# Optimization experiments

Hardware: AMD Instinct MI355X
Metric: run time of the kernel (lower is better)

Reference implementation:

```python
import jax, jax.numpy as jnp
import numpy as np

# Config matching init_kwargs: input_shape=(C,T,H,W)=(512,32,14,14), window_size=9, n_heads=8
B, C, T, H, W = 2, 512, 32, 14, 14
N, K = 8, 9
CI = C // N              # per-head inter channels (64)
P = (K - 1) // 2         # symmetric temporal zero-pad so S == T


def setup_inputs() -> dict:
    key = jax.random.key(0)
    ks = jax.random.split(key, 7)
    s = 0.02
    return {
        "x":  jax.random.normal(ks[0], (B, C, T, H, W), jnp.float32),
        # per-head 1x1x1 conv (Linear3d) weights/biases, stacked over heads
        "Wq": jax.random.normal(ks[1], (N, CI, C), jnp.float32) * s,
        "bq": jax.random.normal(ks[2], (N, CI), jnp.float32) * s,
        "Wk": jax.random.normal(ks[3], (N, CI, C), jnp.float32) * s,
        "bk": jax.random.normal(ks[4], (N, CI), jnp.float32) * s,
        "Wv": jax.random.normal(ks[5], (N, CI, C), jnp.float32) * s,
        "bv": jax.random.normal(ks[6], (N, CI), jnp.float32) * s,
    }


def reference(x, Wq, bq, Wk, bk, Wv, bv):
    # x: (B, C, T, H, W). Dropout (p=0.25) is inference-mode identity.
    Bx, Cx, Tx, Hx, Wd = x.shape
    HW = Hx * Wd
    xf = x.reshape(Bx, Cx, Tx, HW)

    # Queries: every original frame is the center of its own window -> project x directly.
    q = jnp.einsum('bctp,nic->bnitp', xf, Wq) + bq[None, :, :, None, None]  # (B,N,ci,T,HW)

    # Keys/values on temporally zero-padded input (Pad3d gives S == T windows).
    xp = jnp.pad(xf, ((0, 0), (0, 0), (P, P), (0, 0)))  # (B,C,T+K-1,HW)
    k = jnp.einsum('bctp,nic->bnitp', xp, Wk) + bk[None, :, :, None, None]
    v = jnp.einsum('bctp,nic->bnitp', xp, Wv) + bv[None, :, :, None, None]

    # Sliding windows over padded time: window s covers padded frames s..s+K-1
    win = jnp.arange(Tx)[:, None] + jnp.arange(K)[None, :]  # (T,K)
    kw = k[:, :, :, win]  # (B,N,ci,T,K,HW)
    vw = v[:, :, :, win].reshape(Bx, N, CI, Tx, K * HW)

    # alpha[b,n,t,p,m] = sum_i q[b,n,i,t,p] * k_win[b,n,i,t,m]; softmax over keys m
    alpha = jnp.einsum('bnitp,bnitkm->bntpkm', q, kw).reshape(Bx, N, Tx, HW, K * HW)
    alpha = jax.nn.softmax(alpha, axis=-1)

    # y = alpha @ value -> (B,N,ci,T,HW); head concat is channel-major reshape
    y = jnp.einsum('bntpm,bnitm->bnitp', alpha, vw)
    z = y.reshape(Bx, Cx, Tx, Hx, Wd) + x  # residual
    return z
```

## Files before the change

kernel.cpp:

```cpp
#include <hip/hip_runtime.h>
#include <hip/hip_bf16.h>
#include <stdint.h>
#include <cstddef>

#define BB  2
#define CC  512
#define TT  32
#define HWP 196
#define NH  8
#define KWIN 9
#define CID 64
#define PPAD 4
#define TP  40
#define MTOT 12544
#define NTOT 1536
#define VSLOT 224
#define LOG2E 1.44269504f

typedef unsigned short u16;
typedef unsigned int   u32;
typedef __attribute__((ext_vector_type(8))) short short8;
typedef __attribute__((ext_vector_type(4))) float floatx4;

__device__ __forceinline__ u16 f2bf(float f) {
    u32 u = __float_as_uint(f);
    u32 r = (u + 0x7fffu + ((u >> 16) & 1u)) >> 16;
    return (u16)r;
}
__device__ __forceinline__ u32 pack2bf(float a, float b) {
    return (u32)f2bf(a) | ((u32)f2bf(b) << 16);
}
__device__ __forceinline__ u32 packtrunc(float a, float b) {
    return __builtin_amdgcn_perm(__float_as_uint(b), __float_as_uint(a), 0x07060302u);
}
__device__ __forceinline__ float fexp2(float x) {
    return __builtin_amdgcn_exp2f(x);
}
__device__ __forceinline__ void gload16(const u16* g, u16* l) {
    __builtin_amdgcn_global_load_lds(
        (const __attribute__((address_space(1))) u32*)g,
        (__attribute__((address_space(3))) u32*)l, 16, 0, 0);
}

__global__ __launch_bounds__(256) void prep_transpose(
    const float* __restrict__ x, u16* __restrict__ xt,
    const float* __restrict__ Wq, const float* __restrict__ Wk,
    const float* __restrict__ Wv, u16* __restrict__ Wbf,
    const float* __restrict__ bk, const float* __restrict__ bv,
    u16* __restrict__ Kout, u16* __restrict__ Vtp)
{
    __shared__ float T[64 * 197];
    int bxg = blockIdx.x;
    int tid = threadIdx.x;

    if (bxg < BB * TT * 8) {
        int bx = bxg;
        int ct = bx & 7; bx >>= 3;
        int t = bx & 31;
        int b = bx >> 5;
        const float* src = x + ((size_t)(b * CC + ct * 64) * TT + t) * HWP;
        for (int i = tid; i < 64 * 49; i += 256) {
            int c = i / 49;
            int p4 = i - c * 49;
            float4 v = *(const float4*)(src + (size_t)c * (TT * HWP) + p4 * 4);
            float* Tp = &T[c * 197 + p4 * 4];
            Tp[0] = v.x; Tp[1] = v.y; Tp[2] = v.z; Tp[3] = v.w;
        }
        __syncthreads();
        u16* dst = xt + (size_t)((b * TT + t) * HWP) * CC + ct * 64;
        for (int i = tid; i < HWP * 8; i += 256) {
            int p = i >> 3;
            int c0 = (i & 7) * 8;
            u32 w[4];
            #pragma unroll
            for (int k = 0; k < 4; k++)
                w[k] = pack2bf(T[(c0 + 2 * k) * 197 + p],
                               T[(c0 + 2 * k + 1) * 197 + p]);
            *(uint4*)(dst + (size_t)p * CC + c0) = *(uint4*)w;
        }
        return;
    }

    int id = (bxg - BB * TT * 8) * 256 + tid;
    const int wtot = NTOT * CC / 2;
    const int kper = 2 * NH * 8 * HWP * 32;
    const int vper = 2 * NH * 8 * 64 * (VSLOT/2);
    if (id < wtot) {
        int c2 = id & 255;
        int oc = id >> 8;
        int kind = oc >> 9;
        int idx = oc & 511;
        const float* src = (kind == 0 ? Wq : (kind == 1 ? Wk : Wv)) + (size_t)idx * CC + c2 * 2;
        ((u32*)Wbf)[id] = pack2bf(src[0], src[1]);
    } else if (id < wtot + kper) {
        int i = id - wtot;
        int ci2 = i & 31; i >>= 5;
        int p = i % HWP;  i /= HWP;
        int fr = i & 7;   i >>= 3;
        int head = i & 7;
        int b = i >> 3;
        int tp = fr < 4 ? fr : fr + 32;
        const float* bias = bk + head * CID + ci2 * 2;
        size_t addr = (((size_t)(b * NH + head) * TP + tp) * HWP + p) * 32 + ci2;
        ((u32*)Kout)[addr] = pack2bf(bias[0], bias[1]);
    } else if (id < wtot + kper + vper) {
        int i = id - wtot - kper;
        int s2 = i % (VSLOT/2); i /= (VSLOT/2);
        int ci = i & 63; i >>= 6;
        int fr = i & 7;  i >>= 3;
        int head = i & 7;
        int b = i >> 3;
        int tp = fr < 4 ? fr : fr + 32;
        float bias = bv[head * CID + ci];
        size_t addr = (((size_t)(b * NH + head) * TP + tp) * 64 + ci) * (VSLOT/2) + s2;
        ((u32*)Vtp)[addr] = pack2bf(bias, bias);
    }
}

__global__ __launch_bounds__(512) void proj_gemm2(
    const u16* __restrict__ xt, const u16* __restrict__ Wbf,
    const float* __restrict__ bq, const float* __restrict__ bk,
    const float* __restrict__ bv,
    u16* __restrict__ Qout, u16* __restrict__ Kout, u16* __restrict__ Vplain)
{
    __shared__ u16 sA[128 * 64];
    __shared__ u16 sB[256 * 64];

    int bx = blockIdx.x;
    int nb = bx % 6;
    int mt = bx / 6;
    int tid = threadIdx.x;
    int wave = tid >> 6, lane = tid & 63, quad = lane >> 4, l15 = lane & 15;
    int wm = wave >> 2, wn = wave & 3;
    int mbase = mt * 128 + wm * 64;
    int nbase = nb * 256 + wn * 64;

    int lr = lane >> 3;
    int sw = ((lane & 7) * 8) ^ (lr << 3);

    floatx4 acc[4][4];
    #pragma unroll
    for (int ms = 0; ms < 4; ms++)
        #pragma unroll
        for (int ns = 0; ns < 4; ns++)
            acc[ms][ns] = (floatx4){0.f, 0.f, 0.f, 0.f};

    const u16* abase = xt + (size_t)(mt * 128) * CC;
    const u16* bbase = Wbf + (size_t)(nb * 256) * CC;

    for (int kc = 0; kc < 8; kc++) {
        __syncthreads();
        #pragma unroll
        for (int i = 0; i < 2; i++) {
            int rbase = wave * 16 + i * 8;
            gload16(abase + (size_t)(rbase + lr) * CC + kc * 64 + sw,
                    &sA[rbase * 64]);
        }
        #pragma unroll
        for (int i = 0; i < 4; i++) {
            int rbase = wave * 32 + i * 8;
            gload16(bbase + (size_t)(rbase + lr) * CC + kc * 64 + sw,
                    &sB[rbase * 64]);
        }
        __syncthreads();

        #pragma unroll
        for (int kk = 0; kk < 2; kk++) {
            int swr = (kk * 32 + quad * 8) ^ ((l15 & 7) << 3);
            short8 af[4], bf[4];
            #pragma unroll
            for (int ms = 0; ms < 4; ms++)
                af[ms] = *(const short8*)&sA[(wm * 64 + ms * 16 + l15) * 64 + swr];
            #pragma unroll
            for (int ns = 0; ns < 4; ns++)
                bf[ns] = *(const short8*)&sB[(wn * 64 + ns * 16 + l15) * 64 + swr];
            #pragma unroll
            for (int ms = 0; ms < 4; ms++)
                #pragma unroll
                for (int ns = 0; ns < 4; ns++)
                    acc[ms][ns] = __builtin_amdgcn_mfma_f32_16x16x32_bf16(
                        af[ms], bf[ns], acc[ms][ns], 0, 0, 0);
        }
    }

    float biasv[4];
    #pragma unroll
    for (int ns = 0; ns < 4; ns++) {
        int n = nbase + ns * 16 + l15;
        int kind = n >> 9;
        int idx = n & 511;
        const float* bpb = kind == 0 ? bq : (kind == 1 ? bk : bv);
        biasv[ns] = bpb[idx];
    }

    #pragma unroll
    for (int ms = 0; ms < 4; ms++) {
        #pragma unroll
        for (int r = 0; r < 4; r++) {
            int m = mbase + ms * 16 + quad * 4 + r;
            int b = m / (TT * HWP);
            int rem = m - b * (TT * HWP);
            int t = rem / HWP;
            int p = rem - t * HWP;
            #pragma unroll
            for (int ns = 0; ns < 4; ns++) {
                int n = nbase + ns * 16 + l15;
                int kind = n >> 9;
                int idx = n & 511;
                int head = idx >> 6;
                int ci = idx & 63;
                float val = acc[ms][ns][r] + biasv[ns];
                if (kind == 0) {
                    Qout[(((size_t)(b * NH + head) * TT + t) * HWP + p) * CID + ci]
                        = f2bf(val * LOG2E);
                } else if (kind == 1) {
                    Kout[(((size_t)(b * NH + head) * TP + (t + PPAD)) * HWP + p) * CID + ci]
                        = f2bf(val);
                } else {
                    Vplain[(((size_t)(b * NH + head) * TT + t) * HWP + p) * CID + ci]
                        = f2bf(val);
                }
            }
        }
    }
}

__global__ __launch_bounds__(256) void v_reformat(
    const u16* __restrict__ Vplain, u16* __restrict__ Vtp)
{
    __shared__ u16 T[HWP * 66];
    int bx = blockIdx.x;
    int t = bx & 31;
    int slab = bx >> 5;
    int tid = threadIdx.x;
    const u32* src = (const u32*)(Vplain + ((size_t)slab * TT + t) * (HWP * CID));
    for (int i = tid; i < HWP * 32; i += 256) {
        int p = i >> 5, c2 = i & 31;
        u32 v = src[i];
        T[p * 66 + c2 * 2]     = (u16)(v & 0xffffu);
        T[p * 66 + c2 * 2 + 1] = (u16)(v >> 16);
    }
    __syncthreads();
    u32* dst = (u32*)(Vtp + ((size_t)slab * TP + (t + PPAD)) * (64 * VSLOT));
    for (int i = tid; i < 64 * 98; i += 256) {
        int ci = i / 98;
        int s2 = i - ci * 98;
        int s = s2 * 2;
        int s5 = s & 31;
        int p0 = (s & ~31) | (((s5 >> 2) & 1) << 4) | ((s5 >> 3) << 2) | (s5 & 3);
        u32 lo = T[p0 * 66 + ci];
        u32 hi = T[(p0 + 1) * 66 + ci];
        dst[ci * (VSLOT / 2) + s2] = lo | (hi << 16);
    }
}

__global__ __launch_bounds__(256, 1) void attn_mfma4(
    const float* __restrict__ x,
    const u16* __restrict__ Qb, const u16* __restrict__ Kb,
    const u16* __restrict__ Vtp, float* __restrict__ zout)
{
    __shared__ float eT[HWP * 66];

    int i = blockIdx.x;
    int xcd = i & 7;
    int r = i >> 3;
    int slab = ((r >= 32) ? 8 : 0) | xcd;
    int t = r & 31;
    int b = slab >> 3, n = slab & 7;

    int tid = threadIdx.x;
    int wave = tid >> 6;
    int lane = tid & 63;
    int quad = lane >> 4, l15 = lane & 15;

    const u16* kfr0 = Kb + (size_t)slab * (TP * HWP) * CID;
    const u16* vslab = Vtp + (size_t)slab * (TP * 64 * VSLOT);
    const float tmask = (quad == 0) ? 1.0f : 0.0f;

    short8 qf[4][2];
    #pragma unroll
    for (int j = 0; j < 4; j++) {
        int qrow = (wave + 4 * j) * 16 + l15;
        qrow = qrow < HWP ? qrow : (HWP - 1);
        const u16* qp = Qb + ((size_t)(slab * TT + t) * HWP + qrow) * CID;
        qf[j][0] = *(const short8*)(qp + quad * 8);
        qf[j][1] = *(const short8*)(qp + 32 + quad * 8);
    }

    floatx4 acc[4][4];
    floatx4 accl[4];
    #pragma unroll
    for (int j = 0; j < 4; j++) {
        #pragma unroll
        for (int cg = 0; cg < 4; cg++) acc[j][cg] = (floatx4){0.f, 0.f, 0.f, 0.f};
        accl[j] = (floatx4){0.f, 0.f, 0.f, 0.f};
    }

    union { u32 w[4]; short8 s; } ones;
    ones.w[0] = 0x3F803F80u; ones.w[1] = 0x3F803F80u;
    ones.w[2] = 0x3F803F80u; ones.w[3] = 0x3F803F80u;

    #define KLOAD(c, D00, D01, D10, D11) do {                                    \
        const u16* a0_ = kfr0 + (size_t)(rbase + (c) * 32 + l15) * CID + quad * 8;\
        const u16* a1_ = a0_ + (size_t)16 * CID;                                 \
        D00 = *(const short8*)a0_;  D01 = *(const short8*)(a0_ + 32);            \
        D10 = *(const short8*)a1_;  D11 = *(const short8*)(a1_ + 32);            \
    } while (0)

    #define KLOADTAIL(D00, D01) do {                                             \
        int g_ = rbase + 192 + l15;                                              \
        g_ = g_ < (TP * HWP - 1) ? g_ : (TP * HWP - 1);                          \
        const u16* a0_ = kfr0 + (size_t)g_ * CID + quad * 8;                     \
        D00 = *(const short8*)a0_;  D01 = *(const short8*)(a0_ + 32);            \
    } while (0)

    #define VLOAD(c, D0, D1, D2, D3) do {                                        \
        const u16* v_ = vfr + l15 * VSLOT + (c) * 32 + quad * 8;                 \
        D0 = *(const short8*)v_;                                                 \
        D1 = *(const short8*)(v_ + 16 * VSLOT);                                  \
        D2 = *(const short8*)(v_ + 32 * VSLOT);                                  \
        D3 = *(const short8*)(v_ + 48 * VSLOT);                                  \
    } while (0)

    #define CHUNK_FULL(K00, K01, K10, K11, V0, V1, V2, V3) do {                  \
        __builtin_amdgcn_s_setprio(1);                                           \
        _Pragma("unroll")                                                        \
        for (int j = 0; j < 4; j++) {                                            \
            floatx4 sc0 = (floatx4){0.f, 0.f, 0.f, 0.f};                         \
            sc0 = __builtin_amdgcn_mfma_f32_16x16x32_bf16(K00, qf[j][0], sc0, 0, 0, 0); \
            sc0 = __builtin_amdgcn_mfma_f32_16x16x32_bf16(K01, qf[j][1], sc0, 0, 0, 0); \
            floatx4 sc1 = (floatx4){0.f, 0.f, 0.f, 0.f};                         \
            sc1 = __builtin_amdgcn_mfma_f32_16x16x32_bf16(K10, qf[j][0], sc1, 0, 0, 0); \
            sc1 = __builtin_amdgcn_mfma_f32_16x16x32_bf16(K11, qf[j][1], sc1, 0, 0, 0); \
            union { u32 w[4]; short8 s; } pf;                                    \
            pf.w[0] = packtrunc(fexp2(sc0[0]), fexp2(sc0[1]));                   \
            pf.w[1] = packtrunc(fexp2(sc0[2]), fexp2(sc0[3]));                   \
            pf.w[2] = packtrunc(fexp2(sc1[0]), fexp2(sc1[1]));                   \
            pf.w[3] = packtrunc(fexp2(sc1[2]), fexp2(sc1[3]));                   \
            acc[j][0] = __builtin_amdgcn_mfma_f32_16x16x32_bf16(pf.s, V0, acc[j][0], 0, 0, 0); \
            acc[j][1] = __builtin_amdgcn_mfma_f32_16x16x32_bf16(pf.s, V1, acc[j][1], 0, 0, 0); \
            acc[j][2] = __builtin_amdgcn_mfma_f32_16x16x32_bf16(pf.s, V2, acc[j][2], 0, 0, 0); \
            acc[j][3] = __builtin_amdgcn_mfma_f32_16x16x32_bf16(pf.s, V3, acc[j][3], 0, 0, 0); \
            accl[j]   = __builtin_amdgcn_mfma_f32_16x16x32_bf16(pf.s, ones.s, accl[j], 0, 0, 0); \
        }                                                                        \
        __builtin_amdgcn_s_setprio(0);                                           \
    } while (0)

    #define CHUNK_TAIL(K00, K01, V0, V1, V2, V3) do {                            \
        __builtin_amdgcn_s_setprio(1);                                           \
        _Pragma("unroll")                                                        \
        for (int j = 0; j < 4; j++) {                                            \
            floatx4 sc0 = (floatx4){0.f, 0.f, 0.f, 0.f};                         \
            sc0 = __builtin_amdgcn_mfma_f32_16x16x32_bf16(K00, qf[j][0], sc0, 0, 0, 0); \
            sc0 = __builtin_amdgcn_mfma_f32_16x16x32_bf16(K01, qf[j][1], sc0, 0, 0, 0); \
            union { u32 w[4]; short8 s; } pf;                                    \
            pf.w[0] = packtrunc(fexp2(sc0[0]) * tmask, fexp2(sc0[1]) * tmask);   \
            pf.w[1] = packtrunc(fexp2(sc0[2]) * tmask, fexp2(sc0[3]) * tmask);   \
            pf.w[2] = 0u;                                                        \
            pf.w[3] = 0u;                                                        \
            acc[j][0] = __builtin_amdgcn_mfma_f32_16x16x32_bf16(pf.s, V0, acc[j][0], 0, 0, 0); \
            acc[j][1] = __builtin_amdgcn_mfma_f32_16x16x32_bf16(pf.s, V1, acc[j][1], 0, 0, 0); \
            acc[j][2] = __builtin_amdgcn_mfma_f32_16x16x32_bf16(pf.s, V2, acc[j][2], 0, 0, 0); \
            acc[j][3] = __builtin_amdgcn_mfma_f32_16x16x32_bf16(pf.s, V3, acc[j][3], 0, 0, 0); \
            accl[j]   = __builtin_amdgcn_mfma_f32_16x16x32_bf16(pf.s, ones.s, accl[j], 0, 0, 0); \
        }                                                                        \
        __builtin_amdgcn_s_setprio(0);                                           \
    } while (0)

    for (int f = 0; f < KWIN; f++) {
        int rbase = (t + f) * HWP;
        const u16* vfr = vslab + (size_t)(t + f) * (64 * VSLOT);

        short8 ka00, ka01, ka10, ka11, va0, va1, va2, va3;
        short8 kb00, kb01, kb10, kb11, vb0, vb1, vb2, vb3;
        short8 kc00, kc01, kc10, kc11, vc0, vc1, vc2, vc3;

        KLOAD(0, ka00, ka01, ka10, ka11);  VLOAD(0, va0, va1, va2, va3);
        KLOAD(1, kb00, kb01, kb10, kb11);  VLOAD(1, vb0, vb1, vb2, vb3);
        KLOAD(2, kc00, kc01, kc10, kc11);  VLOAD(2, vc0, vc1, vc2, vc3);
        CHUNK_FULL(ka00, ka01, ka10, ka11, va0, va1, va2, va3);
        KLOAD(3, ka00, ka01, ka10, ka11);  VLOAD(3, va0, va1, va2, va3);
        CHUNK_FULL(kb00, kb01, kb10, kb11, vb0, vb1, vb2, vb3);
        KLOAD(4, kb00, kb01, kb10, kb11);  VLOAD(4, vb0, vb1, vb2, vb3);
        CHUNK_FULL(kc00, kc01, kc10, kc11, vc0, vc1, vc2, vc3);
        KLOAD(5, kc00, kc01, kc10, kc11);  VLOAD(5, vc0, vc1, vc2, vc3);
        CHUNK_FULL(ka00, ka01, ka10, ka11, va0, va1, va2, va3);
        KLOADTAIL(ka00, ka01);             VLOAD(6, va0, va1, va2, va3);
        CHUNK_FULL(kb00, kb01, kb10, kb11, vb0, vb1, vb2, vb3);
        CHUNK_FULL(kc00, kc01, kc10, kc11, vc0, vc1, vc2, vc3);
        CHUNK_TAIL(ka00, ka01, va0, va1, va2, va3);
    }

    #undef KLOAD
    #undef KLOADTAIL
    #undef VLOAD
    #undef CHUNK_FULL
    #undef CHUNK_TAIL

    #pragma unroll
    for (int j = 0; j < 4; j++) {
        int tg = wave + 4 * j;
        float il[4];
        #pragma unroll
        for (int rr = 0; rr < 4; rr++) il[rr] = 1.0f / accl[j][rr];
        #pragma unroll
        for (int cg = 0; cg < 4; cg++) {
            #pragma unroll
            for (int rr = 0; rr < 4; rr++) {
                int p = tg * 16 + quad * 4 + rr;
                if (p < HWP)
                    eT[p * 66 + cg * 16 + l15] = acc[j][cg][rr] * il[rr];
            }
        }
    }
    __syncthreads();

    if (tid < HWP) {
        size_t base = ((size_t)(b * CC + n * CID) * TT + t) * HWP + tid;
        for (int ci = 0; ci < 64; ci++) {
            size_t a = base + (size_t)ci * (TT * HWP);
            zout[a] = eT[tid * 66 + ci] + x[a];
        }
    }
}

extern "C" void kernel_launch(void* const* d_in, const int* in_sizes, int n_in,
                              void* d_out, int out_size, void* d_ws, size_t ws_size,
                              hipStream_t stream) {
    const float* x  = (const float*)d_in[0];
    const float* Wq = (const float*)d_in[1];
    const float* bq = (const float*)d_in[2];
    const float* Wk = (const float*)d_in[3];
    const float* bk = (const float*)d_in[4];
    const float* Wv = (const float*)d_in[5];
    const float* bv = (const float*)d_in[6];
    float* z = (float*)d_out;

    const size_t qElems   = (size_t)BB * NH * TT * HWP * CID;
    const size_t kElems   = (size_t)BB * NH * TP * HWP * CID;
    const size_t vtpElems = (size_t)BB * NH * TP * 64 * VSLOT;

    u16* Qw  = (u16*)d_ws;
    u16* Kw  = Qw + qElems;
    u16* Vtp = Kw + kElems;
    u16* Wb  = Vtp + vtpElems;
    u16* Xt  = (u16*)d_out;
    u16* Vpl = Xt + qElems;

    {
        const int wtot = NTOT * CC / 2;
        const int kper = 2 * NH * 8 * HWP * 32;
        const int vper = 2 * NH * 8 * 64 * (VSLOT / 2);
        const int prepBlocks = (wtot + kper + vper + 255) / 256;
        prep_transpose<<<BB * TT * 8 + prepBlocks, 256, 0, stream>>>(
            x, Xt, Wq, Wk, Wv, Wb, bk, bv, Kw, Vtp);
    }
    proj_gemm2<<<98 * 6, 512, 0, stream>>>(Xt, Wb, bq, bk, bv, Qw, Kw, Vpl);
    v_reformat<<<BB * NH * TT, 256, 0, stream>>>(Vpl, Vtp);
    attn_mfma4<<<512, 256, 0, stream>>>(x, Qw, Kw, Vtp, z);
}
```

Before: 243.6 us.

## Fuse V reformat into projection epilogue and drop setprio in attention chunks

The projection GEMM now writes V directly into the permuted transposed slot layout the attention kernel consumes, computing the slot index per row, so the separate v_reformat kernel and its intermediate buffer go away. That removes one launch and a full read/write pass over V. In exchange, the V stores from the GEMM epilogue are strided by VSLOT and poorly coalesced. Separately, the s_setprio raise/lower around the MFMA chunks in the attention kernel is removed and the macros no longer use do/while wrappers.

```diff
diff --git a/kernel.cpp b/kernel.cpp
--- a/kernel.cpp
+++ b/kernel.cpp
@@ -121,7 +121,7 @@
     const u16* __restrict__ xt, const u16* __restrict__ Wbf,
     const float* __restrict__ bq, const float* __restrict__ bk,
     const float* __restrict__ bv,
-    u16* __restrict__ Qout, u16* __restrict__ Kout, u16* __restrict__ Vplain)
+    u16* __restrict__ Qout, u16* __restrict__ Kout, u16* __restrict__ Vtp)
 {
     __shared__ u16 sA[128 * 64];
     __shared__ u16 sB[256 * 64];
@@ -202,6 +202,8 @@
             int rem = m - b * (TT * HWP);
             int t = rem / HWP;
             int p = rem - t * HWP;
+            int slot_p = (p & ~31) | (p & 3) | (((p >> 4) & 1) << 2)
+                       | (((p >> 2) & 1) << 3) | (((p >> 3) & 1) << 4);
             #pragma unroll
             for (int ns = 0; ns < 4; ns++) {
                 int n = nbase + ns * 16 + l15;
@@ -217,40 +219,11 @@
                     Kout[(((size_t)(b * NH + head) * TP + (t + PPAD)) * HWP + p) * CID + ci]
                         = f2bf(val);
                 } else {
-                    Vplain[(((size_t)(b * NH + head) * TT + t) * HWP + p) * CID + ci]
+                    Vtp[(((size_t)(b * NH + head) * TP + (t + PPAD)) * 64 + ci) * VSLOT + slot_p]
                         = f2bf(val);
                 }
             }
         }
-    }
-}
-
-__global__ __launch_bounds__(256) void v_reformat(
-    const u16* __restrict__ Vplain, u16* __restrict__ Vtp)
-{
-    __shared__ u16 T[HWP * 66];
-    int bx = blockIdx.x;
-    int t = bx & 31;
-    int slab = bx >> 5;
-    int tid = threadIdx.x;
-    const u32* src = (const u32*)(Vplain + ((size_t)slab * TT + t) * (HWP * CID));
-    for (int i = tid; i < HWP * 32; i += 256) {
-        int p = i >> 5, c2 = i & 31;
-        u32 v = src[i];
-        T[p * 66 + c2 * 2]     = (u16)(v & 0xffffu);
-        T[p * 66 + c2 * 2 + 1] = (u16)(v >> 16);
-    }
-    __syncthreads();
-    u32* dst = (u32*)(Vtp + ((size_t)slab * TP + (t + PPAD)) * (64 * VSLOT));
-    for (int i = tid; i < 64 * 98; i += 256) {
-        int ci = i / 98;
-        int s2 = i - ci * 98;
-        int s = s2 * 2;
-        int s5 = s & 31;
-        int p0 = (s & ~31) | (((s5 >> 2) & 1) << 4) | ((s5 >> 3) << 2) | (s5 & 3);
-        u32 lo = T[p0 * 66 + ci];
-        u32 hi = T[(p0 + 1) * 66 + ci];
-        dst[ci * (VSLOT / 2) + s2] = lo | (hi << 16);
     }
 }
 
@@ -322,8 +295,7 @@
         D3 = *(const short8*)(v_ + 48 * VSLOT);                                  \
     } while (0)
 
-    #define CHUNK_FULL(K00, K01, K10, K11, V0, V1, V2, V3) do {                  \
-        __builtin_amdgcn_s_setprio(1);                                           \
+    #define CHUNK_FULL(K00, K01, K10, K11, V0, V1, V2, V3)                       \
         _Pragma("unroll")                                                        \
         for (int j = 0; j < 4; j++) {                                            \
             floatx4 sc0 = (floatx4){0.f, 0.f, 0.f, 0.f};                         \
@@ -342,12 +314,9 @@
             acc[j][2] = __builtin_amdgcn_mfma_f32_16x16x32_bf16(pf.s, V2, acc[j][2], 0, 0, 0); \
             acc[j][3] = __builtin_amdgcn_mfma_f32_16x16x32_bf16(pf.s, V3, acc[j][3], 0, 0, 0); \
             accl[j]   = __builtin_amdgcn_mfma_f32_16x16x32_bf16(pf.s, ones.s, accl[j], 0, 0, 0); \
-        }                                                                        \
-        __builtin_amdgcn_s_setprio(0);                                           \
-    } while (0)
-
-    #define CHUNK_TAIL(K00, K01, V0, V1, V2, V3) do {                            \
-        __builtin_amdgcn_s_setprio(1);                                           \
+        }
+
+    #define CHUNK_TAIL(K00, K01, V0, V1, V2, V3)                                 \
         _Pragma("unroll")                                                        \
         for (int j = 0; j < 4; j++) {                                            \
             floatx4 sc0 = (floatx4){0.f, 0.f, 0.f, 0.f};                         \
@@ -363,9 +332,7 @@
             acc[j][2] = __builtin_amdgcn_mfma_f32_16x16x32_bf16(pf.s, V2, acc[j][2], 0, 0, 0); \
             acc[j][3] = __builtin_amdgcn_mfma_f32_16x16x32_bf16(pf.s, V3, acc[j][3], 0, 0, 0); \
             accl[j]   = __builtin_amdgcn_mfma_f32_16x16x32_bf16(pf.s, ones.s, accl[j], 0, 0, 0); \
-        }                                                                        \
-        __builtin_amdgcn_s_setprio(0);                                           \
-    } while (0)
+        }
 
     for (int f = 0; f < KWIN; f++) {
         int rbase = (t + f) * HWP;
@@ -445,7 +412,6 @@
     u16* Vtp = Kw + kElems;
     u16* Wb  = Vtp + vtpElems;
     u16* Xt  = (u16*)d_out;
-    u16* Vpl = Xt + qElems;
 
     {
         const int wtot = NTOT * CC / 2;
@@ -455,7 +421,6 @@
         prep_transpose<<<BB * TT * 8 + prepBlocks, 256, 0, stream>>>(
             x, Xt, Wq, Wk, Wv, Wb, bk, bv, Kw, Vtp);
     }
-    proj_gemm2<<<98 * 6, 512, 0, stream>>>(Xt, Wb, bq, bk, bv, Qw, Kw, Vpl);
-    v_reformat<<<BB * NH * TT, 256, 0, stream>>>(Vpl, Vtp);
+    proj_gemm2<<<98 * 6, 512, 0, stream>>>(Xt, Wb, bq, bk, bv, Qw, Kw, Vtp);
     attn_mfma4<<<512, 256, 0, stream>>>(x, Qw, Kw, Vtp, z);
 }
```

Result: no change. 242.0 us (-0.6%).
